# Kernel optimization log

Measured on AMD Instinct MI355X. Metric: run time of the kernel, lower is better.

## Reference

```python
import jax, jax.numpy as jnp
import numpy as np

B, L, IN, H, T = 512, 16, 128, 1024, 64


def setup_inputs() -> dict:
    key = jax.random.key(0)
    ks = jax.random.split(key, 11)
    k = 1.0 / np.sqrt(H)  # torch default init scale
    u = lambda kk, shape: jax.random.uniform(kk, shape, jnp.float32, -k, k)
    return {
        "x": jax.random.normal(ks[0], (B, L, IN), jnp.float32),
        "W_ih0": u(ks[1], (4 * H, IN)),
        "W_hh0": u(ks[2], (4 * H, H)),
        "b_ih0": u(ks[3], (4 * H,)),
        "b_hh0": u(ks[4], (4 * H,)),
        "W_ih1": u(ks[5], (4 * H, H)),
        "W_hh1": u(ks[6], (4 * H, H)),
        "b_ih1": u(ks[7], (4 * H,)),
        "b_hh1": u(ks[8], (4 * H,)),
        "W_out": u(ks[9], (IN, H)),
        "b_out": u(ks[10], (IN,)),
        "t": T,
    }


def _cell(xt, h, c, W_ih, W_hh, b_ih, b_hh):
    # PyTorch LSTM cell; gate order i, f, g, o
    g = xt @ W_ih.T + h @ W_hh.T + (b_ih + b_hh)
    i, f, gg, o = jnp.split(g, 4, axis=-1)
    c = jax.nn.sigmoid(f) * c + jax.nn.sigmoid(i) * jnp.tanh(gg)
    h = jax.nn.sigmoid(o) * jnp.tanh(c)
    return h, c


def reference(x, W_ih0, W_hh0, b_ih0, b_hh0, W_ih1, W_hh1, b_ih1, b_hh1,
              W_out, b_out, t):
    layers = ((W_ih0, W_hh0, b_ih0, b_hh0), (W_ih1, W_hh1, b_ih1, b_hh1))
    Bn = x.shape[0]
    Hn = W_hh0.shape[1]

    def stack_step(state, xt):
        new_state = []
        inp = xt
        for (h, c), p in zip(state, layers):
            h, c = _cell(inp, h, c, *p)
            new_state.append((h, c))
            inp = h
        return tuple(new_state), inp  # inp = top-layer hidden [B, H]

    z = jnp.zeros((Bn, Hn), x.dtype)
    state0 = tuple((z, z) for _ in layers)

    # prompt phase: process x over time, keep final state and last top hidden
    state, tops = jax.lax.scan(stack_step, state0, x.transpose(1, 0, 2))
    x_last = x[:, -1] + (tops[-1] @ W_out.T + b_out)  # [B, IN]

    def gen_step(carry, _):
        st, xl = carry
        st, htop = stack_step(st, xl)
        xl = xl + (htop @ W_out.T + b_out)
        return (st, xl), xl

    (_, _), gen = jax.lax.scan(gen_step, (state, x_last), None, length=t - 1)

    out = jnp.concatenate(
        [x, x_last[:, None, :], gen.transpose(1, 0, 2)], axis=1
    )  # [B, L + t, IN]
    return out
```

## Files before the change

kernel.cpp:

```cpp
#include <hip/hip_runtime.h>

#define B_    512
#define L_    16
#define IN_   128
#define H_    1024
#define T_    64
#define OUTROW 10240

#define LDC   1040
#define LDXL  144
#define RSTRIDE 67
#define RSZ   (64 * RSTRIDE)

#define KH_X  64
#define KH_H  32
#define KH_XL 4
#define KH_W0 36
#define KH_W1 64
#define KH_WO 32

typedef __attribute__((ext_vector_type(8))) short bf8;
typedef __attribute__((ext_vector_type(4))) float f4;
typedef __attribute__((ext_vector_type(4))) unsigned short us4;
typedef unsigned short u16;
typedef unsigned int   u32;

#define MFMA16(a, b, c) __builtin_amdgcn_mfma_f32_16x16x32_bf16(a, b, c, 0, 0, 0)

__device__ __forceinline__ u16 f2bf(float f) {
    u32 u = __builtin_bit_cast(u32, f);
    u32 r = (u + 0x7fffu + ((u >> 16) & 1u)) >> 16;
    return (u16)r;
}
__device__ __forceinline__ float sigm(float x) { return 1.f / (1.f + __expf(-x)); }
__device__ __forceinline__ float tanh_f(float x) {
    float ax = fabsf(x);
    float e = __expf(-2.f * ax);
    float t = (1.f - e) / (1.f + e);
    return x < 0.f ? -t : t;
}
__device__ __forceinline__ bf8 ld8(const u16* p) { return *(const bf8*)p; }

__device__ __forceinline__ size_t swz(int kh_stride, int row, int k) {
    return ((size_t)(row >> 4) * kh_stride + (k >> 5)) * 512
           + ((k & 31) >> 3) * 128 + (row & 15) * 8 + (k & 7);
}

#define MFMAP(AS, BS)                                                       \
  do {                                                                      \
    _Pragma("unroll")                                                       \
    for (int g_ = 0; g_ < 4; ++g_)                                          \
      _Pragma("unroll")                                                     \
      for (int t_ = 0; t_ < 4; ++t_)                                        \
        acc[g_][t_] = MFMA16(AS[g_], BS[t_], acc[g_][t_]);                  \
  } while (0)

#define LOADP_CELL(AS, BS, PH)                                              \
  do {                                                                      \
    const int kt_ = ws + (((PH) >> 1) << 2);                                \
    const int s_  = (PH) & 1;                                               \
    const bool ix_ = kt_ < nk1;                                             \
    const int oA_ = (((ix_ ? kt_ : kt_ - nk1) << 1) + s_) * 512;            \
    const int oB_ = ((kt_ << 1) + s_) * 512;                                \
    _Pragma("unroll")                                                       \
    for (int g_ = 0; g_ < 4; ++g_)                                          \
      AS[g_] = ld8((ix_ ? apx[g_] : aph[g_]) + oA_);                        \
    _Pragma("unroll")                                                       \
    for (int t_ = 0; t_ < 4; ++t_) BS[t_] = ld8(bp[t_] + oB_);              \
  } while (0)

#define LOADP_PROJ(AS, BS, PH)                                              \
  do {                                                                      \
    const int kt_ = ws + (((PH) >> 1) << 2);                                \
    const int o_  = ((kt_ << 1) + ((PH) & 1)) * 512;                        \
    _Pragma("unroll")                                                       \
    for (int g_ = 0; g_ < 4; ++g_) AS[g_] = ld8(ap[g_] + o_);               \
    _Pragma("unroll")                                                       \
    for (int t_ = 0; t_ < 4; ++t_) BS[t_] = ld8(bp[t_] + o_);               \
  } while (0)

__device__ __forceinline__ void cell_body(int bid,
    const u16* __restrict__ pA0, int kh0, int nk1,
    const u16* __restrict__ pA1, int kh1, int nk2,
    const u16* __restrict__ pB, int khB,
    const float* __restrict__ bias, float* __restrict__ Cst,
    u16* __restrict__ Hdst, float* __restrict__ red)
{
    const int tn = (bid & 7) * 8 + ((bid >> 3) & 7);
    const int tm = bid >> 6;
    const int tid = threadIdx.x;
    const int lane = tid & 63, ws = tid >> 6;
    const int l15 = lane & 15, qd = lane >> 4, q4 = qd * 4;

    const int erow = ws * 16 + l15;
    const int grow = tm * 64 + erow;
    const int colb = tn * 16 + q4;
    const f4 cold = *(const f4*)&Cst[(size_t)grow * LDC + colb];

    f4 acc[4][4];
#pragma unroll
    for (int i = 0; i < 4; ++i)
#pragma unroll
        for (int j = 0; j < 4; ++j) acc[i][j] = (f4)(0.f);

    const u16* bp[4];
#pragma unroll
    for (int t = 0; t < 4; ++t)
        bp[t] = pB + (size_t)(tn * 4 + t) * khB * 512 + lane * 8;
    const u16* apx[4];
    const u16* aph[4];
#pragma unroll
    for (int g = 0; g < 4; ++g) {
        apx[g] = pA0 + (size_t)(tm * 4 + g) * kh0 * 512 + lane * 8;
        aph[g] = pA1 + (size_t)(tm * 4 + g) * kh1 * 512 + lane * 8;
    }

    const int nk  = nk1 + nk2;
    const int myn = (nk - ws + 3) >> 2;
    const int nph = myn * 2;

    bf8 A0[4], B0[4], A1[4], B1[4], A2[4], B2[4], A3[4], B3[4];
    LOADP_CELL(A0, B0, 0);
    LOADP_CELL(A1, B1, 1);
    LOADP_CELL(A2, B2, 2);
    int ph = 0;
    for (; ph + 4 <= nph; ph += 4) {
        LOADP_CELL(A3, B3, ph + 3);
        MFMAP(A0, B0);
        if (ph + 4 < nph) LOADP_CELL(A0, B0, ph + 4);
        MFMAP(A1, B1);
        if (ph + 5 < nph) LOADP_CELL(A1, B1, ph + 5);
        MFMAP(A2, B2);
        if (ph + 6 < nph) LOADP_CELL(A2, B2, ph + 6);
        MFMAP(A3, B3);
    }
    if (ph < nph) {
        MFMAP(A0, B0);
        MFMAP(A1, B1);
    }

#pragma unroll
    for (int rg = 0; rg < 4; ++rg)
#pragma unroll
        for (int t = 0; t < 4; ++t)
#pragma unroll
            for (int r = 0; r < 4; ++r)
                red[ws * RSZ + (rg * 16 + q4 + r) * RSTRIDE + t * 16 + l15] = acc[rg][t][r];
    __syncthreads();

    f4 gs[4];
#pragma unroll
    for (int G = 0; G < 4; ++G) {
        f4 s;
#pragma unroll
        for (int j = 0; j < 4; ++j) {
            const int cidx = erow * RSTRIDE + G * 16 + q4 + j;
            s[j] = red[0 * RSZ + cidx] + red[1 * RSZ + cidx]
                 + red[2 * RSZ + cidx] + red[3 * RSZ + cidx];
        }
        gs[G] = s + *(const f4*)&bias[tn * 64 + G * 16 + q4];
    }
    f4 cn; us4 h4;
#pragma unroll
    for (int j = 0; j < 4; ++j) {
        const float I  = sigm(gs[0][j]);
        const float F  = sigm(gs[1][j]);
        const float Gg = tanh_f(gs[2][j]);
        const float O  = sigm(gs[3][j]);
        cn[j] = F * cold[j] + I * Gg;
        h4[j] = f2bf(O * tanh_f(cn[j]));
    }
    *(f4*)&Cst[(size_t)grow * LDC + colb] = cn;
    *(us4*)&Hdst[swz(KH_H, grow, colb)] = h4;
}

__global__ __launch_bounds__(256, 2) void cell_gemm(
    const u16* __restrict__ pA0, int kh0, int nk1,
    const u16* __restrict__ pA1, int kh1, int nk2,
    const u16* __restrict__ pB, int khB,
    const float* __restrict__ bias, float* __restrict__ Cst, u16* __restrict__ Hdst)
{
    __shared__ float red[4 * RSZ];
    cell_body(blockIdx.x, pA0, kh0, nk1, pA1, kh1, nk2, pB, khB, bias, Cst, Hdst, red);
}

__global__ __launch_bounds__(256, 2) void pair_k(
    const u16* __restrict__ A0a, int kh0a, int nk1a,
    const u16* __restrict__ A1a, int kh1a, int nk2a,
    const u16* __restrict__ Ba, int khBa,
    const float* __restrict__ ba, float* __restrict__ Ca, u16* __restrict__ Ha,
    const u16* __restrict__ A0b, int kh0b, int nk1b,
    const u16* __restrict__ A1b, int kh1b, int nk2b,
    const u16* __restrict__ Bb, int khBb,
    const float* __restrict__ bb, float* __restrict__ Cb, u16* __restrict__ Hb)
{
    __shared__ float red[4 * RSZ];
    if (blockIdx.x < 512)
        cell_body(blockIdx.x, A0a, kh0a, nk1a, A1a, kh1a, nk2a, Ba, khBa, ba, Ca, Ha, red);
    else
        cell_body(blockIdx.x - 512, A0b, kh0b, nk1b, A1b, kh1b, nk2b, Bb, khBb, bb, Cb, Hb, red);
}

__global__ __launch_bounds__(256, 2) void proj_gemm(
    const u16* __restrict__ pA,
    const u16* __restrict__ pB,
    const float* __restrict__ bout,
    const float* __restrict__ xin, int ldxin,
    float* __restrict__ XL, u16* __restrict__ XLbf,
    float* __restrict__ dout, int slot)
{
    __shared__ float red[4 * RSZ];
    const int bid = blockIdx.x;
    const int tn = bid >> 3, tm = bid & 7;
    const int tid = threadIdx.x;
    const int lane = tid & 63, ws = tid >> 6;
    const int l15 = lane & 15, qd = lane >> 4;

    f4 acc[4][4];
#pragma unroll
    for (int i = 0; i < 4; ++i)
#pragma unroll
        for (int j = 0; j < 4; ++j) acc[i][j] = (f4)(0.f);

    const u16* bp[4];
#pragma unroll
    for (int t = 0; t < 4; ++t)
        bp[t] = pB + (size_t)(tn * 4 + t) * KH_WO * 512 + lane * 8;
    const u16* ap[4];
#pragma unroll
    for (int g = 0; g < 4; ++g)
        ap[g] = pA + (size_t)(tm * 4 + g) * KH_H * 512 + lane * 8;

    const int nph = 8;
    bf8 A0[4], B0[4], A1[4], B1[4], A2[4], B2[4], A3[4], B3[4];
    LOADP_PROJ(A0, B0, 0);
    LOADP_PROJ(A1, B1, 1);
    LOADP_PROJ(A2, B2, 2);
    for (int ph = 0; ph + 4 <= nph; ph += 4) {
        LOADP_PROJ(A3, B3, ph + 3);
        MFMAP(A0, B0);
        if (ph + 4 < nph) LOADP_PROJ(A0, B0, ph + 4);
        MFMAP(A1, B1);
        if (ph + 5 < nph) LOADP_PROJ(A1, B1, ph + 5);
        MFMAP(A2, B2);
        if (ph + 6 < nph) LOADP_PROJ(A2, B2, ph + 6);
        MFMAP(A3, B3);
    }

#pragma unroll
    for (int rg = 0; rg < 4; ++rg)
#pragma unroll
        for (int t = 0; t < 4; ++t)
#pragma unroll
            for (int r = 0; r < 4; ++r)
                red[ws * RSZ + (rg * 16 + qd * 4 + r) * RSTRIDE + t * 16 + l15] = acc[rg][t][r];
    __syncthreads();

    const int erow = ws * 16 + l15;
    const int grow = tm * 64 + erow;
#pragma unroll
    for (int jb = 0; jb < 4; ++jb) {
        const int cin = qd * 16 + jb * 4;
        const int col = tn * 64 + cin;
        f4 s;
#pragma unroll
        for (int j2 = 0; j2 < 4; ++j2) {
            const int cidx = erow * RSTRIDE + cin + j2;
            s[j2] = red[0 * RSZ + cidx] + red[1 * RSZ + cidx]
                  + red[2 * RSZ + cidx] + red[3 * RSZ + cidx];
        }
        const f4 v = *(const f4*)&xin[(size_t)grow * ldxin + col] + s
                     + *(const f4*)&bout[col];
        *(f4*)&XL[(size_t)grow * LDXL + col] = v;
        us4 b;
#pragma unroll
        for (int j2 = 0; j2 < 4; ++j2) b[j2] = f2bf(v[j2]);
        *(us4*)&XLbf[swz(KH_XL, grow, col)] = b;
        *(f4*)&dout[(size_t)grow * OUTROW + slot * IN_ + col] = v;
    }
}

__global__ void conv_w(const float* Wih0, const float* Whh0, const float* bih0, const float* bhh0,
                       const float* Wih1, const float* Whh1, const float* bih1, const float* bhh1,
                       const float* Wout,
                       u16* W0c, float* b0p, u16* W1c, float* b1p, u16* Woutb)
{
    const int bid = blockIdx.x, t = threadIdx.x;
    const int lane = t >> 2;
    const int l15 = lane & 15, qd = lane >> 4;
    const int j0 = (t & 3) * 2;
    const int c0_ = qd * 8 + j0;

    if (bid < 9216) {
        const int rg = bid / 36, kh = bid - rg * 36;
        const int p = rg * 16 + l15;
        const int rem = p & 63, G = rem >> 4, u = (p >> 6) * 16 + (rem & 15);
        const int src = G * H_ + u;
        float e0, e1;
        if (kh < 4) {
            e0 = Wih0[(size_t)src * IN_ + kh * 32 + c0_];
            e1 = Wih0[(size_t)src * IN_ + kh * 32 + c0_ + 1];
        } else {
            e0 = Whh0[(size_t)src * H_ + (kh - 4) * 32 + c0_];
            e1 = Whh0[(size_t)src * H_ + (kh - 4) * 32 + c0_ + 1];
        }
        ((u32*)W0c)[(size_t)bid * 256 + t] = (u32)f2bf(e0) | ((u32)f2bf(e1) << 16);
        if (kh == 0 && qd == 0 && j0 == 0) b0p[p] = bih0[src] + bhh0[src];
    } else if (bid < 25600) {
        const int x = bid - 9216;
        const int rg = x >> 6, kh = x & 63;
        const int p = rg * 16 + l15;
        const int rem = p & 63, G = rem >> 4, u = (p >> 6) * 16 + (rem & 15);
        const int src = G * H_ + u;
        float e0, e1;
        if (kh < 32) {
            e0 = Wih1[(size_t)src * H_ + kh * 32 + c0_];
            e1 = Wih1[(size_t)src * H_ + kh * 32 + c0_ + 1];
        } else {
            e0 = Whh1[(size_t)src * H_ + (kh - 32) * 32 + c0_];
            e1 = Whh1[(size_t)src * H_ + (kh - 32) * 32 + c0_ + 1];
        }
        ((u32*)W1c)[(size_t)x * 256 + t] = (u32)f2bf(e0) | ((u32)f2bf(e1) << 16);
        if (kh == 0 && qd == 0 && j0 == 0) b1p[p] = bih1[src] + bhh1[src];
    } else {
        const int x = bid - 25600;
        const int rg = x >> 5, kh = x & 31;
        const int r = rg * 16 + l15;
        const float e0 = Wout[(size_t)r * H_ + kh * 32 + c0_];
        const float e1 = Wout[(size_t)r * H_ + kh * 32 + c0_ + 1];
        ((u32*)Woutb)[(size_t)x * 256 + t] = (u32)f2bf(e0) | ((u32)f2bf(e1) << 16);
    }
}

__global__ void setup_k(const float* __restrict__ x, u16* __restrict__ Xb,
                        u16* H0, u16* H1, float* c0, float* c1,
                        float* __restrict__ dout)
{
    const int i = blockIdx.x * 256 + threadIdx.x;
    const float v = x[i];
    const int r = i >> 11, col = i & 2047;
    Xb[swz(KH_X, r, col)] = f2bf(v);
    dout[(size_t)r * OUTROW + col] = v;
    if (i < B_ * H_) {
        H0[i] = 0; H1[i] = 0;
        const int rr = i >> 10, cc = i & 1023;
        c0[(size_t)rr * LDC + cc] = 0.f; c1[(size_t)rr * LDC + cc] = 0.f;
    }
}

extern "C" void kernel_launch(void* const* d_in, const int* in_sizes, int n_in,
                              void* d_out, int out_size, void* d_ws, size_t ws_size,
                              hipStream_t stream)
{
    const float* x    = (const float*)d_in[0];
    const float* Wih0 = (const float*)d_in[1];
    const float* Whh0 = (const float*)d_in[2];
    const float* bih0 = (const float*)d_in[3];
    const float* bhh0 = (const float*)d_in[4];
    const float* Wih1 = (const float*)d_in[5];
    const float* Whh1 = (const float*)d_in[6];
    const float* bih1 = (const float*)d_in[7];
    const float* bhh1 = (const float*)d_in[8];
    const float* Wout = (const float*)d_in[9];
    const float* bout = (const float*)d_in[10];
    float* dout = (float*)d_out;

    char* ws = (char*)d_ws;
    size_t off = 0;
    auto alloc = [&](size_t bytes) -> char* {
        char* p = ws + off; off += (bytes + 255) & ~(size_t)255; return p;
    };
    u16*  W0c   = (u16*)alloc((size_t)9216 * 1024);
    u16*  W1c   = (u16*)alloc((size_t)16384 * 1024);
    u16*  Woutb = (u16*)alloc((size_t)256 * 1024);
    float* b0p  = (float*)alloc(4096 * 4);
    float* b1p  = (float*)alloc(4096 * 4);
    u16*  Xb    = (u16*)alloc((size_t)2048 * 1024);
    u16*  H0b[2]; H0b[0] = (u16*)alloc((size_t)1024 * 1024); H0b[1] = (u16*)alloc((size_t)1024 * 1024);
    u16*  H1b[2]; H1b[0] = (u16*)alloc((size_t)1024 * 1024); H1b[1] = (u16*)alloc((size_t)1024 * 1024);
    float* c0   = (float*)alloc((size_t)B_ * LDC * 4);
    float* c1   = (float*)alloc((size_t)B_ * LDC * 4);
    float* XL   = (float*)alloc((size_t)B_ * LDXL * 4);
    u16*  XLbf  = (u16*)alloc((size_t)128 * 1024);

    conv_w<<<25856, 256, 0, stream>>>(Wih0, Whh0, bih0, bhh0,
                                      Wih1, Whh1, bih1, bhh1, Wout,
                                      W0c, b0p, W1c, b1p, Woutb);
    setup_k<<<4096, 256, 0, stream>>>(x, Xb, H0b[0], H1b[0], c0, c1, dout);

    int p = 0;
    cell_gemm<<<512, 256, 0, stream>>>(Xb, KH_X, 2, H0b[0], KH_H, 16,
                                       W0c, KH_W0, b0p, c0, H0b[1]);
    for (int g = 0; g < 15; ++g) {
        pair_k<<<1024, 256, 0, stream>>>(
            H0b[1 - p], KH_H, 16, H1b[p], KH_H, 16, W1c, KH_W1, b1p, c1, H1b[1 - p],
            Xb + (size_t)(g + 1) * 2048, KH_X, 2, H0b[1 - p], KH_H, 16,
            W0c, KH_W0, b0p, c0, H0b[p]);
        p ^= 1;
    }
    cell_gemm<<<512, 256, 0, stream>>>(H0b[0], KH_H, 16, H1b[1], KH_H, 16,
                                       W1c, KH_W1, b1p, c1, H1b[0]);
    proj_gemm<<<16, 256, 0, stream>>>(H1b[0], Woutb, bout,
                                      x + 15 * IN_, L_ * IN_, XL, XLbf, dout, 16);

    p = 0;
    for (int g = 16; g < 79; ++g) {
        cell_gemm<<<512, 256, 0, stream>>>(XLbf, KH_XL, 2, H0b[p], KH_H, 16,
                                           W0c, KH_W0, b0p, c0, H0b[1 - p]);
        cell_gemm<<<512, 256, 0, stream>>>(H0b[1 - p], KH_H, 16, H1b[p], KH_H, 16,
                                           W1c, KH_W1, b1p, c1, H1b[1 - p]);
        const int s = g - 15;
        proj_gemm<<<16, 256, 0, stream>>>(H1b[1 - p], Woutb, bout,
                                          XL, LDXL, XL, XLbf, dout, 16 + s);
        p ^= 1;
    }
}
```

Measured before the change: 2.623 ms.

## Fuse layer-1 cell and output projection into one kernel with per-row-tile counters

Merges the layer-1 LSTM cell GEMM and the output projection into one launch. The 64 projection blocks spin on per-row-tile atomic counters until the 64 cell blocks producing that tile's hidden state have finished. The projection is also re-tiled from 16 blocks with 64x64 tiles into 64 blocks with 16x64 tiles, giving more parallelism and a smaller register footprint. This saves a launch and a serial tail each step. The risks are spin-wait deadlock if the spinning blocks take CUs before the producer blocks run, and memory-ordering hazards.

Result: slower. 3.355 ms (+27.9%).

```diff
diff --git a/kernel.cpp b/kernel.cpp
--- a/kernel.cpp
+++ b/kernel.cpp
@@ -11,6 +11,7 @@
 #define LDXL  144
 #define RSTRIDE 67
 #define RSZ   (64 * RSTRIDE)
+#define PRST  68
 
 #define KH_X  64
 #define KH_H  32
@@ -69,22 +70,12 @@
     for (int t_ = 0; t_ < 4; ++t_) BS[t_] = ld8(bp[t_] + oB_);              \
   } while (0)
 
-#define LOADP_PROJ(AS, BS, PH)                                              \
-  do {                                                                      \
-    const int kt_ = ws + (((PH) >> 1) << 2);                                \
-    const int o_  = ((kt_ << 1) + ((PH) & 1)) * 512;                        \
-    _Pragma("unroll")                                                       \
-    for (int g_ = 0; g_ < 4; ++g_) AS[g_] = ld8(ap[g_] + o_);               \
-    _Pragma("unroll")                                                       \
-    for (int t_ = 0; t_ < 4; ++t_) BS[t_] = ld8(bp[t_] + o_);               \
-  } while (0)
-
 __device__ __forceinline__ void cell_body(int bid,
     const u16* __restrict__ pA0, int kh0, int nk1,
     const u16* __restrict__ pA1, int kh1, int nk2,
     const u16* __restrict__ pB, int khB,
     const float* __restrict__ bias, float* __restrict__ Cst,
-    u16* __restrict__ Hdst, float* __restrict__ red)
+    u16* Hdst, float* __restrict__ red)
 {
     const int tn = (bid & 7) * 8 + ((bid >> 3) & 7);
     const int tm = bid >> 6;
@@ -201,83 +192,101 @@
         cell_body(blockIdx.x - 512, A0b, kh0b, nk1b, A1b, kh1b, nk2b, Bb, khBb, bb, Cb, Hb, red);
 }
 
-__global__ __launch_bounds__(256, 2) void proj_gemm(
-    const u16* __restrict__ pA,
+__global__ __launch_bounds__(256, 2) void fused_k(
+    const u16* __restrict__ pA0, const u16* __restrict__ pA1,
     const u16* __restrict__ pB,
+    const float* __restrict__ bias, float* __restrict__ Cst, u16* Hdst,
+    const u16* pH1,
+    const u16* __restrict__ pWo,
     const float* __restrict__ bout,
     const float* __restrict__ xin, int ldxin,
     float* __restrict__ XL, u16* __restrict__ XLbf,
-    float* __restrict__ dout, int slot)
+    float* __restrict__ dout, int slot,
+    u32* cnt, u32 target)
 {
     __shared__ float red[4 * RSZ];
     const int bid = blockIdx.x;
-    const int tn = bid >> 3, tm = bid & 7;
     const int tid = threadIdx.x;
+
+    if (bid < 512) {
+        cell_body(bid, pA0, KH_H, 16, pA1, KH_H, 16, pB, KH_W1,
+                  bias, Cst, Hdst, red);
+        __syncthreads();
+        if (tid == 0) {
+            __threadfence();
+            atomicAdd(&cnt[(bid >> 6) * 32], 1u);
+        }
+        return;
+    }
+
+    const int pb = bid - 512;
+    const int tn = pb & 1, tmq = pb >> 1;
+    const int tm = tmq >> 2;
     const int lane = tid & 63, ws = tid >> 6;
     const int l15 = lane & 15, qd = lane >> 4;
 
-    f4 acc[4][4];
-#pragma unroll
-    for (int i = 0; i < 4; ++i)
-#pragma unroll
-        for (int j = 0; j < 4; ++j) acc[i][j] = (f4)(0.f);
-
+    if (tid == 0) {
+        while (__hip_atomic_load(&cnt[tm * 32], __ATOMIC_ACQUIRE,
+                                 __HIP_MEMORY_SCOPE_AGENT) < target)
+            __builtin_amdgcn_s_sleep(8);
+        __threadfence();
+    }
+    __syncthreads();
+
+    f4 acc[4];
+#pragma unroll
+    for (int t = 0; t < 4; ++t) acc[t] = (f4)(0.f);
+
+    const u16* ap = pH1 + (size_t)tmq * KH_H * 512 + lane * 8;
     const u16* bp[4];
 #pragma unroll
     for (int t = 0; t < 4; ++t)
-        bp[t] = pB + (size_t)(tn * 4 + t) * KH_WO * 512 + lane * 8;
-    const u16* ap[4];
-#pragma unroll
-    for (int g = 0; g < 4; ++g)
-        ap[g] = pA + (size_t)(tm * 4 + g) * KH_H * 512 + lane * 8;
-
-    const int nph = 8;
-    bf8 A0[4], B0[4], A1[4], B1[4], A2[4], B2[4], A3[4], B3[4];
-    LOADP_PROJ(A0, B0, 0);
-    LOADP_PROJ(A1, B1, 1);
-    LOADP_PROJ(A2, B2, 2);
-    for (int ph = 0; ph + 4 <= nph; ph += 4) {
-        LOADP_PROJ(A3, B3, ph + 3);
-        MFMAP(A0, B0);
-        if (ph + 4 < nph) LOADP_PROJ(A0, B0, ph + 4);
-        MFMAP(A1, B1);
-        if (ph + 5 < nph) LOADP_PROJ(A1, B1, ph + 5);
-        MFMAP(A2, B2);
-        if (ph + 6 < nph) LOADP_PROJ(A2, B2, ph + 6);
-        MFMAP(A3, B3);
-    }
-
-#pragma unroll
-    for (int rg = 0; rg < 4; ++rg)
-#pragma unroll
-        for (int t = 0; t < 4; ++t)
-#pragma unroll
-            for (int r = 0; r < 4; ++r)
-                red[ws * RSZ + (rg * 16 + qd * 4 + r) * RSTRIDE + t * 16 + l15] = acc[rg][t][r];
+        bp[t] = pWo + (size_t)(tn * 4 + t) * KH_WO * 512 + lane * 8;
+
+    bf8 A0, B0[4], A1, B1[4];
+#define LOADP_P(AV, BV, PH)                                                 \
+    do {                                                                    \
+        const int kt_ = ws + (((PH) >> 1) << 2);                            \
+        const int o_  = ((kt_ << 1) + ((PH) & 1)) * 512;                    \
+        AV = ld8(ap + o_);                                                  \
+        _Pragma("unroll")                                                   \
+        for (int t_ = 0; t_ < 4; ++t_) BV[t_] = ld8(bp[t_] + o_);           \
+    } while (0)
+
+    LOADP_P(A0, B0, 0);
+    for (int ph = 0; ph < 8; ph += 2) {
+        LOADP_P(A1, B1, ph + 1);
+#pragma unroll
+        for (int t = 0; t < 4; ++t) acc[t] = MFMA16(A0, B0[t], acc[t]);
+        if (ph + 2 < 8) LOADP_P(A0, B0, ph + 2);
+#pragma unroll
+        for (int t = 0; t < 4; ++t) acc[t] = MFMA16(A1, B1[t], acc[t]);
+    }
+#undef LOADP_P
+
+#pragma unroll
+    for (int t = 0; t < 4; ++t)
+#pragma unroll
+        for (int r = 0; r < 4; ++r)
+            red[ws * (16 * PRST) + (qd * 4 + r) * PRST + t * 16 + l15] = acc[t][r];
     __syncthreads();
 
-    const int erow = ws * 16 + l15;
-    const int grow = tm * 64 + erow;
-#pragma unroll
-    for (int jb = 0; jb < 4; ++jb) {
-        const int cin = qd * 16 + jb * 4;
-        const int col = tn * 64 + cin;
-        f4 s;
-#pragma unroll
-        for (int j2 = 0; j2 < 4; ++j2) {
-            const int cidx = erow * RSTRIDE + cin + j2;
-            s[j2] = red[0 * RSZ + cidx] + red[1 * RSZ + cidx]
-                  + red[2 * RSZ + cidx] + red[3 * RSZ + cidx];
-        }
-        const f4 v = *(const f4*)&xin[(size_t)grow * ldxin + col] + s
-                     + *(const f4*)&bout[col];
-        *(f4*)&XL[(size_t)grow * LDXL + col] = v;
-        us4 b;
-#pragma unroll
-        for (int j2 = 0; j2 < 4; ++j2) b[j2] = f2bf(v[j2]);
-        *(us4*)&XLbf[swz(KH_XL, grow, col)] = b;
-        *(f4*)&dout[(size_t)grow * OUTROW + slot * IN_ + col] = v;
-    }
+    const int row = tid >> 4;
+    const int cq  = (tid & 15) * 4;
+    const int col = tn * 64 + cq;
+    const int grow = tmq * 16 + row;
+    f4 s = (f4)(0.f);
+#pragma unroll
+    for (int w = 0; w < 4; ++w)
+        s += *(const f4*)&red[w * (16 * PRST) + row * PRST + cq];
+    const f4 v = *(const f4*)&xin[(size_t)grow * ldxin + col] + s
+                 + *(const f4*)&bout[col];
+    *(f4*)&XL[(size_t)grow * LDXL + col] = v;
+    us4 b;
+#pragma unroll
+    for (int j = 0; j < 4; ++j) b[j] = f2bf(v[j]);
+    *(us4*)&XLbf[swz(KH_XL, grow, col)] = b;
+    *(f4*)&dout[(size_t)grow * OUTROW + slot * IN_ + col] = v;
 }
 
 __global__ void conv_w(const float* Wih0, const float* Whh0, const float* bih0, const float* bhh0,
@@ -334,9 +343,10 @@
 
 __global__ void setup_k(const float* __restrict__ x, u16* __restrict__ Xb,
                         u16* H0, u16* H1, float* c0, float* c1,
-                        float* __restrict__ dout)
+                        float* __restrict__ dout, u32* cnt)
 {
     const int i = blockIdx.x * 256 + threadIdx.x;
+    if (i < 256) cnt[i] = 0;
     const float v = x[i];
     const int r = i >> 11, col = i & 2047;
     Xb[swz(KH_X, r, col)] = f2bf(v);
@@ -382,11 +392,12 @@
     float* c1   = (float*)alloc((size_t)B_ * LDC * 4);
     float* XL   = (float*)alloc((size_t)B_ * LDXL * 4);
     u16*  XLbf  = (u16*)alloc((size_t)128 * 1024);
+    u32*  cnt   = (u32*)alloc(256 * 4);
 
     conv_w<<<25856, 256, 0, stream>>>(Wih0, Whh0, bih0, bhh0,
                                       Wih1, Whh1, bih1, bhh1, Wout,
                                       W0c, b0p, W1c, b1p, Woutb);
-    setup_k<<<4096, 256, 0, stream>>>(x, Xb, H0b[0], H1b[0], c0, c1, dout);
+    setup_k<<<4096, 256, 0, stream>>>(x, Xb, H0b[0], H1b[0], c0, c1, dout, cnt);
 
     int p = 0;
     cell_gemm<<<512, 256, 0, stream>>>(Xb, KH_X, 2, H0b[0], KH_H, 16,
@@ -398,20 +409,20 @@
             W0c, KH_W0, b0p, c0, H0b[p]);
         p ^= 1;
     }
-    cell_gemm<<<512, 256, 0, stream>>>(H0b[0], KH_H, 16, H1b[1], KH_H, 16,
-                                       W1c, KH_W1, b1p, c1, H1b[0]);
-    proj_gemm<<<16, 256, 0, stream>>>(H1b[0], Woutb, bout,
-                                      x + 15 * IN_, L_ * IN_, XL, XLbf, dout, 16);
+    fused_k<<<576, 256, 0, stream>>>(H0b[0], H1b[1], W1c, b1p, c1, H1b[0],
+                                     H1b[0], Woutb, bout,
+                                     x + 15 * IN_, L_ * IN_, XL, XLbf, dout, 16,
+                                     cnt, 64u * 1);
 
     p = 0;
     for (int g = 16; g < 79; ++g) {
         cell_gemm<<<512, 256, 0, stream>>>(XLbf, KH_XL, 2, H0b[p], KH_H, 16,
                                            W0c, KH_W0, b0p, c0, H0b[1 - p]);
-        cell_gemm<<<512, 256, 0, stream>>>(H0b[1 - p], KH_H, 16, H1b[p], KH_H, 16,
-                                           W1c, KH_W1, b1p, c1, H1b[1 - p]);
         const int s = g - 15;
-        proj_gemm<<<16, 256, 0, stream>>>(H1b[1 - p], Woutb, bout,
-                                          XL, LDXL, XL, XLbf, dout, 16 + s);
+        fused_k<<<576, 256, 0, stream>>>(H0b[1 - p], H1b[p], W1c, b1p, c1, H1b[1 - p],
+                                         H1b[1 - p], Woutb, bout,
+                                         XL, LDXL, XL, XLbf, dout, 16 + s,
+                                         cnt, 64u * (u32)(s + 1));
         p ^= 1;
     }
 }
```

## Fold output projection into layer-0 input via precomputed Wih0·Wout and running preactivation

Applied to the files above, without the earlier changes.

Layer 0's input-gate preactivation during rollout is kept as a running fp32 buffer P. Because x_last grows by W_out·h_top + b_out each step, P is advanced by (Wih0·Wout)·h_top + Wih0·b_out, using a combined weight precomputed once. The standalone projection GEMM is folded into the layer-0 cell kernel, where 2 of 64 column tiles compute it, and the small-K XL input GEMM is removed. This cuts one launch per step and shortens the dependency chain, but adds a 4096x1024 combined-weight GEMM operand, a P read-modify-write, and bf16 rounding of the combined weight, which may change accuracy.

New measurement: 3.250 ms. 23.9% more time.

```diff
diff --git a/kernel.cpp b/kernel.cpp
--- a/kernel.cpp
+++ b/kernel.cpp
@@ -9,12 +9,12 @@
 
 #define LDC   1040
 #define LDXL  144
+#define LDP   4112
 #define RSTRIDE 67
 #define RSZ   (64 * RSTRIDE)
 
 #define KH_X  64
 #define KH_H  32
-#define KH_XL 4
 #define KH_W0 36
 #define KH_W1 64
 #define KH_WO 32
@@ -46,14 +46,15 @@
            + ((k & 31) >> 3) * 128 + (row & 15) * 8 + (k & 7);
 }
 
-#define MFMAP(AS, BS)                                                       \
+#define MFMAPX(ACC, AS, BS)                                                 \
   do {                                                                      \
     _Pragma("unroll")                                                       \
     for (int g_ = 0; g_ < 4; ++g_)                                          \
       _Pragma("unroll")                                                     \
       for (int t_ = 0; t_ < 4; ++t_)                                        \
-        acc[g_][t_] = MFMA16(AS[g_], BS[t_], acc[g_][t_]);                  \
+        ACC[g_][t_] = MFMA16(AS[g_], BS[t_], ACC[g_][t_]);                  \
   } while (0)
+#define MFMAP(AS, BS) MFMAPX(acc, AS, BS)
 
 #define LOADP_CELL(AS, BS, PH)                                              \
   do {                                                                      \
@@ -67,16 +68,6 @@
       AS[g_] = ld8((ix_ ? apx[g_] : aph[g_]) + oA_);                        \
     _Pragma("unroll")                                                       \
     for (int t_ = 0; t_ < 4; ++t_) BS[t_] = ld8(bp[t_] + oB_);              \
-  } while (0)
-
-#define LOADP_PROJ(AS, BS, PH)                                              \
-  do {                                                                      \
-    const int kt_ = ws + (((PH) >> 1) << 2);                                \
-    const int o_  = ((kt_ << 1) + ((PH) & 1)) * 512;                        \
-    _Pragma("unroll")                                                       \
-    for (int g_ = 0; g_ < 4; ++g_) AS[g_] = ld8(ap[g_] + o_);               \
-    _Pragma("unroll")                                                       \
-    for (int t_ = 0; t_ < 4; ++t_) BS[t_] = ld8(bp[t_] + o_);               \
   } while (0)
 
 __device__ __forceinline__ void cell_body(int bid,
@@ -201,83 +192,244 @@
         cell_body(blockIdx.x - 512, A0b, kh0b, nk1b, A1b, kh1b, nk2b, Bb, khBb, bb, Cb, Hb, red);
 }
 
-__global__ __launch_bounds__(256, 2) void proj_gemm(
-    const u16* __restrict__ pA,
-    const u16* __restrict__ pB,
-    const float* __restrict__ bout,
-    const float* __restrict__ xin, int ldxin,
-    float* __restrict__ XL, u16* __restrict__ XLbf,
-    float* __restrict__ dout, int slot)
+__global__ __launch_bounds__(256, 2) void cellA_k(
+    const u16* __restrict__ pH1, const u16* __restrict__ pH0,
+    const u16* __restrict__ pWc, const u16* __restrict__ pW0,
+    const float* __restrict__ b0p_, const float* __restrict__ bc0,
+    float* __restrict__ P, float* __restrict__ Cst, u16* __restrict__ Hdst,
+    const u16* __restrict__ pWo, const float* __restrict__ bout_,
+    float* __restrict__ XL, float* __restrict__ dout, int slot)
 {
     __shared__ float red[4 * RSZ];
     const int bid = blockIdx.x;
-    const int tn = bid >> 3, tm = bid & 7;
+    const int tn = (bid & 7) * 8 + ((bid >> 3) & 7);
+    const int tm = bid >> 6;
     const int tid = threadIdx.x;
     const int lane = tid & 63, ws = tid >> 6;
-    const int l15 = lane & 15, qd = lane >> 4;
-
-    f4 acc[4][4];
-#pragma unroll
-    for (int i = 0; i < 4; ++i)
-#pragma unroll
-        for (int j = 0; j < 4; ++j) acc[i][j] = (f4)(0.f);
-
-    const u16* bp[4];
-#pragma unroll
-    for (int t = 0; t < 4; ++t)
-        bp[t] = pB + (size_t)(tn * 4 + t) * KH_WO * 512 + lane * 8;
-    const u16* ap[4];
-#pragma unroll
-    for (int g = 0; g < 4; ++g)
-        ap[g] = pA + (size_t)(tm * 4 + g) * KH_H * 512 + lane * 8;
-
-    const int nph = 8;
-    bf8 A0[4], B0[4], A1[4], B1[4], A2[4], B2[4], A3[4], B3[4];
-    LOADP_PROJ(A0, B0, 0);
-    LOADP_PROJ(A1, B1, 1);
-    LOADP_PROJ(A2, B2, 2);
-    for (int ph = 0; ph + 4 <= nph; ph += 4) {
-        LOADP_PROJ(A3, B3, ph + 3);
-        MFMAP(A0, B0);
-        if (ph + 4 < nph) LOADP_PROJ(A0, B0, ph + 4);
-        MFMAP(A1, B1);
-        if (ph + 5 < nph) LOADP_PROJ(A1, B1, ph + 5);
-        MFMAP(A2, B2);
-        if (ph + 6 < nph) LOADP_PROJ(A2, B2, ph + 6);
-        MFMAP(A3, B3);
-    }
-
-#pragma unroll
-    for (int rg = 0; rg < 4; ++rg)
-#pragma unroll
-        for (int t = 0; t < 4; ++t)
-#pragma unroll
-            for (int r = 0; r < 4; ++r)
-                red[ws * RSZ + (rg * 16 + qd * 4 + r) * RSTRIDE + t * 16 + l15] = acc[rg][t][r];
-    __syncthreads();
+    const int l15 = lane & 15, qd = lane >> 4, q4 = qd * 4;
 
     const int erow = ws * 16 + l15;
     const int grow = tm * 64 + erow;
-#pragma unroll
-    for (int jb = 0; jb < 4; ++jb) {
-        const int cin = qd * 16 + jb * 4;
-        const int col = tn * 64 + cin;
+    const int colb = tn * 16 + q4;
+    const f4 cold = *(const f4*)&Cst[(size_t)grow * LDC + colb];
+
+    if (tn < 2) {
+        f4 pacc[4][4];
+#pragma unroll
+        for (int i = 0; i < 4; ++i)
+#pragma unroll
+            for (int j = 0; j < 4; ++j) pacc[i][j] = (f4)(0.f);
+        const u16* pap[4];
+        const u16* pbp[4];
+#pragma unroll
+        for (int g = 0; g < 4; ++g)
+            pap[g] = pH1 + (size_t)(tm * 4 + g) * (KH_H * 512) + lane * 8;
+#pragma unroll
+        for (int t = 0; t < 4; ++t)
+            pbp[t] = pWo + (size_t)(tn * 4 + t) * (KH_WO * 512) + lane * 8;
+#define LOADQ(AS, BS, PH)                                                   \
+  { const int o_ = (((ws + (((PH) >> 1) << 2)) << 1) + ((PH) & 1)) * 512;   \
+    _Pragma("unroll")                                                       \
+    for (int g_ = 0; g_ < 4; ++g_) AS[g_] = ld8(pap[g_] + o_);              \
+    _Pragma("unroll")                                                       \
+    for (int t_ = 0; t_ < 4; ++t_) BS[t_] = ld8(pbp[t_] + o_); }
+        bf8 A0[4], B0[4], A1[4], B1[4];
+        LOADQ(A0, B0, 0);
+        for (int ph = 0; ph < 8; ph += 2) {
+            LOADQ(A1, B1, ph + 1);
+            MFMAPX(pacc, A0, B0);
+            if (ph + 2 < 8) LOADQ(A0, B0, ph + 2);
+            MFMAPX(pacc, A1, B1);
+        }
+#undef LOADQ
+#pragma unroll
+        for (int rg = 0; rg < 4; ++rg)
+#pragma unroll
+            for (int t = 0; t < 4; ++t)
+#pragma unroll
+                for (int r = 0; r < 4; ++r)
+                    red[ws * RSZ + (rg * 16 + q4 + r) * RSTRIDE + t * 16 + l15] = pacc[rg][t][r];
+        __syncthreads();
+#pragma unroll
+        for (int jb = 0; jb < 4; ++jb) {
+            const int cin = qd * 16 + jb * 4;
+            const int col = tn * 64 + cin;
+            f4 s;
+#pragma unroll
+            for (int j2 = 0; j2 < 4; ++j2) {
+                const int cidx = erow * RSTRIDE + cin + j2;
+                s[j2] = red[0 * RSZ + cidx] + red[1 * RSZ + cidx]
+                      + red[2 * RSZ + cidx] + red[3 * RSZ + cidx];
+            }
+            const f4 v = *(const f4*)&XL[(size_t)grow * LDXL + col] + s
+                         + *(const f4*)&bout_[col];
+            *(f4*)&XL[(size_t)grow * LDXL + col] = v;
+            *(f4*)&dout[(size_t)grow * OUTROW + slot * IN_ + col] = v;
+        }
+        __syncthreads();
+    }
+
+    const int half = ws >> 1, wl = ws & 1;
+    const u16* ap[4];
+    const u16* bp[4];
+#pragma unroll
+    for (int g = 0; g < 4; ++g)
+        ap[g] = (half ? pH0 : pH1) + (size_t)(tm * 4 + g) * (KH_H * 512) + lane * 8;
+#pragma unroll
+    for (int t = 0; t < 4; ++t)
+        bp[t] = half ? pW0 + (size_t)(tn * 4 + t) * (KH_W0 * 512) + 4 * 512 + lane * 8
+                     : pWc + (size_t)(tn * 4 + t) * (KH_H * 512) + lane * 8;
+
+    f4 acc[4][4];
+#pragma unroll
+    for (int i = 0; i < 4; ++i)
+#pragma unroll
+        for (int j = 0; j < 4; ++j) acc[i][j] = (f4)(0.f);
+
+#define LOADA(AS, BS, PH)                                                   \
+  { const int kt_ = wl + (((PH) >> 1) << 1);                                \
+    const int o_ = ((kt_ << 1) + ((PH) & 1)) * 512;                         \
+    _Pragma("unroll")                                                       \
+    for (int g_ = 0; g_ < 4; ++g_) AS[g_] = ld8(ap[g_] + o_);               \
+    _Pragma("unroll")                                                       \
+    for (int t_ = 0; t_ < 4; ++t_) BS[t_] = ld8(bp[t_] + o_); }
+
+    bf8 A0[4], B0[4], A1[4], B1[4], A2[4], B2[4], A3[4], B3[4];
+    LOADA(A0, B0, 0);
+    LOADA(A1, B1, 1);
+    LOADA(A2, B2, 2);
+    for (int ph = 0; ph + 4 <= 16; ph += 4) {
+        LOADA(A3, B3, ph + 3);
+        MFMAP(A0, B0);
+        if (ph + 4 < 16) LOADA(A0, B0, ph + 4);
+        MFMAP(A1, B1);
+        if (ph + 5 < 16) LOADA(A1, B1, ph + 5);
+        MFMAP(A2, B2);
+        if (ph + 6 < 16) LOADA(A2, B2, ph + 6);
+        MFMAP(A3, B3);
+    }
+#undef LOADA
+
+#pragma unroll
+    for (int rg = 0; rg < 4; ++rg)
+#pragma unroll
+        for (int t = 0; t < 4; ++t)
+#pragma unroll
+            for (int r = 0; r < 4; ++r)
+                red[ws * RSZ + (rg * 16 + q4 + r) * RSTRIDE + t * 16 + l15] = acc[rg][t][r];
+    __syncthreads();
+
+    f4 gs[4];
+#pragma unroll
+    for (int G = 0; G < 4; ++G) {
+        f4 pinc, hp;
+#pragma unroll
+        for (int j = 0; j < 4; ++j) {
+            const int cidx = erow * RSTRIDE + G * 16 + q4 + j;
+            pinc[j] = red[0 * RSZ + cidx] + red[1 * RSZ + cidx];
+            hp[j]   = red[2 * RSZ + cidx] + red[3 * RSZ + cidx];
+        }
+        const int pc = tn * 64 + G * 16 + q4;
+        const f4 pold = *(const f4*)&P[(size_t)grow * LDP + pc];
+        const f4 pnew = pold + pinc + *(const f4*)&bc0[pc];
+        *(f4*)&P[(size_t)grow * LDP + pc] = pnew;
+        gs[G] = pnew + hp + *(const f4*)&b0p_[pc];
+    }
+    f4 cn; us4 h4;
+#pragma unroll
+    for (int j = 0; j < 4; ++j) {
+        const float I  = sigm(gs[0][j]);
+        const float F  = sigm(gs[1][j]);
+        const float Gg = tanh_f(gs[2][j]);
+        const float O  = sigm(gs[3][j]);
+        cn[j] = F * cold[j] + I * Gg;
+        h4[j] = f2bf(O * tanh_f(cn[j]));
+    }
+    *(f4*)&Cst[(size_t)grow * LDC + colb] = cn;
+    *(us4*)&Hdst[swz(KH_H, grow, colb)] = h4;
+}
+
+__global__ __launch_bounds__(256, 2) void pinit_k(
+    const u16* __restrict__ pXb, const u16* __restrict__ pW0,
+    float* __restrict__ P)
+{
+    __shared__ float red[4 * RSZ];
+    const int bid = blockIdx.x;
+    const int tn = (bid & 7) * 8 + ((bid >> 3) & 7);
+    const int tm = bid >> 6;
+    const int tid = threadIdx.x;
+    const int lane = tid & 63, ws = tid >> 6;
+    const int l15 = lane & 15, qd = lane >> 4, q4 = qd * 4;
+
+    f4 acc[4][4];
+#pragma unroll
+    for (int i = 0; i < 4; ++i)
+#pragma unroll
+        for (int j = 0; j < 4; ++j) acc[i][j] = (f4)(0.f);
+
+    bf8 A[4], B[4];
+#pragma unroll
+    for (int g = 0; g < 4; ++g)
+        A[g] = ld8(pXb + ((size_t)(tm * 4 + g) * KH_X + 60 + ws) * 512 + lane * 8);
+#pragma unroll
+    for (int t = 0; t < 4; ++t)
+        B[t] = ld8(pW0 + ((size_t)(tn * 4 + t) * KH_W0 + ws) * 512 + lane * 8);
+    MFMAP(A, B);
+
+#pragma unroll
+    for (int rg = 0; rg < 4; ++rg)
+#pragma unroll
+        for (int t = 0; t < 4; ++t)
+#pragma unroll
+            for (int r = 0; r < 4; ++r)
+                red[ws * RSZ + (rg * 16 + q4 + r) * RSTRIDE + t * 16 + l15] = acc[rg][t][r];
+    __syncthreads();
+
+    const int erow = ws * 16 + l15;
+    const int grow = tm * 64 + erow;
+#pragma unroll
+    for (int G = 0; G < 4; ++G) {
         f4 s;
 #pragma unroll
-        for (int j2 = 0; j2 < 4; ++j2) {
-            const int cidx = erow * RSTRIDE + cin + j2;
-            s[j2] = red[0 * RSZ + cidx] + red[1 * RSZ + cidx]
-                  + red[2 * RSZ + cidx] + red[3 * RSZ + cidx];
-        }
-        const f4 v = *(const f4*)&xin[(size_t)grow * ldxin + col] + s
-                     + *(const f4*)&bout[col];
-        *(f4*)&XL[(size_t)grow * LDXL + col] = v;
-        us4 b;
-#pragma unroll
-        for (int j2 = 0; j2 < 4; ++j2) b[j2] = f2bf(v[j2]);
-        *(us4*)&XLbf[swz(KH_XL, grow, col)] = b;
-        *(f4*)&dout[(size_t)grow * OUTROW + slot * IN_ + col] = v;
-    }
+        for (int j = 0; j < 4; ++j) {
+            const int cidx = erow * RSTRIDE + G * 16 + q4 + j;
+            s[j] = red[0 * RSZ + cidx] + red[1 * RSZ + cidx]
+                 + red[2 * RSZ + cidx] + red[3 * RSZ + cidx];
+        }
+        *(f4*)&P[(size_t)grow * LDP + tn * 64 + G * 16 + q4] = s;
+    }
+}
+
+__global__ void wcomb_k(const float* __restrict__ Wih0, const float* __restrict__ Wout,
+                        u16* __restrict__ Wc)
+{
+    const int idx = blockIdx.x * 256 + threadIdx.x;
+    const int h = idx & 1023, p0 = (idx >> 10) << 2;
+    const int rem = p0 & 63, G = rem >> 4, u0 = (p0 >> 6) * 16 + (rem & 15);
+    const int src0 = G * H_ + u0;
+    float s0 = 0.f, s1 = 0.f, s2 = 0.f, s3 = 0.f;
+    for (int i = 0; i < IN_; ++i) {
+        const float wv = Wout[(size_t)i * H_ + h];
+        s0 += wv * Wih0[(size_t)(src0 + 0) * IN_ + i];
+        s1 += wv * Wih0[(size_t)(src0 + 1) * IN_ + i];
+        s2 += wv * Wih0[(size_t)(src0 + 2) * IN_ + i];
+        s3 += wv * Wih0[(size_t)(src0 + 3) * IN_ + i];
+    }
+    Wc[swz(KH_H, p0 + 0, h)] = f2bf(s0);
+    Wc[swz(KH_H, p0 + 1, h)] = f2bf(s1);
+    Wc[swz(KH_H, p0 + 2, h)] = f2bf(s2);
+    Wc[swz(KH_H, p0 + 3, h)] = f2bf(s3);
+}
+
+__global__ void bc0_k(const float* __restrict__ Wih0, const float* __restrict__ bout_,
+                      float* __restrict__ bc0)
+{
+    const int p = blockIdx.x * 256 + threadIdx.x;
+    const int rem = p & 63, G = rem >> 4, u = (p >> 6) * 16 + (rem & 15);
+    const int src = G * H_ + u;
+    float s = 0.f;
+    for (int i = 0; i < IN_; ++i) s += bout_[i] * Wih0[(size_t)src * IN_ + i];
+    bc0[p] = s;
 }
 
 __global__ void conv_w(const float* Wih0, const float* Whh0, const float* bih0, const float* bhh0,
@@ -334,13 +486,14 @@
 
 __global__ void setup_k(const float* __restrict__ x, u16* __restrict__ Xb,
                         u16* H0, u16* H1, float* c0, float* c1,
-                        float* __restrict__ dout)
+                        float* __restrict__ dout, float* __restrict__ XL)
 {
     const int i = blockIdx.x * 256 + threadIdx.x;
     const float v = x[i];
     const int r = i >> 11, col = i & 2047;
     Xb[swz(KH_X, r, col)] = f2bf(v);
     dout[(size_t)r * OUTROW + col] = v;
+    if (col >= 1920) XL[(size_t)r * LDXL + col - 1920] = v;
     if (i < B_ * H_) {
         H0[i] = 0; H1[i] = 0;
         const int rr = i >> 10, cc = i & 1023;
@@ -373,20 +526,25 @@
     u16*  W0c   = (u16*)alloc((size_t)9216 * 1024);
     u16*  W1c   = (u16*)alloc((size_t)16384 * 1024);
     u16*  Woutb = (u16*)alloc((size_t)256 * 1024);
+    u16*  Wcomb = (u16*)alloc((size_t)8192 * 1024);
     float* b0p  = (float*)alloc(4096 * 4);
     float* b1p  = (float*)alloc(4096 * 4);
+    float* bc0  = (float*)alloc(4096 * 4);
     u16*  Xb    = (u16*)alloc((size_t)2048 * 1024);
     u16*  H0b[2]; H0b[0] = (u16*)alloc((size_t)1024 * 1024); H0b[1] = (u16*)alloc((size_t)1024 * 1024);
     u16*  H1b[2]; H1b[0] = (u16*)alloc((size_t)1024 * 1024); H1b[1] = (u16*)alloc((size_t)1024 * 1024);
     float* c0   = (float*)alloc((size_t)B_ * LDC * 4);
     float* c1   = (float*)alloc((size_t)B_ * LDC * 4);
     float* XL   = (float*)alloc((size_t)B_ * LDXL * 4);
-    u16*  XLbf  = (u16*)alloc((size_t)128 * 1024);
+    float* P    = (float*)alloc((size_t)B_ * LDP * 4);
 
     conv_w<<<25856, 256, 0, stream>>>(Wih0, Whh0, bih0, bhh0,
                                       Wih1, Whh1, bih1, bhh1, Wout,
                                       W0c, b0p, W1c, b1p, Woutb);
-    setup_k<<<4096, 256, 0, stream>>>(x, Xb, H0b[0], H1b[0], c0, c1, dout);
+    wcomb_k<<<4096, 256, 0, stream>>>(Wih0, Wout, Wcomb);
+    bc0_k<<<16, 256, 0, stream>>>(Wih0, bout, bc0);
+    setup_k<<<4096, 256, 0, stream>>>(x, Xb, H0b[0], H1b[0], c0, c1, dout, XL);
+    pinit_k<<<512, 256, 0, stream>>>(Xb, W0c, P);
 
     int p = 0;
     cell_gemm<<<512, 256, 0, stream>>>(Xb, KH_X, 2, H0b[0], KH_H, 16,
@@ -400,18 +558,14 @@
     }
     cell_gemm<<<512, 256, 0, stream>>>(H0b[0], KH_H, 16, H1b[1], KH_H, 16,
                                        W1c, KH_W1, b1p, c1, H1b[0]);
-    proj_gemm<<<16, 256, 0, stream>>>(H1b[0], Woutb, bout,
-                                      x + 15 * IN_, L_ * IN_, XL, XLbf, dout, 16);
-
-    p = 0;
-    for (int g = 16; g < 79; ++g) {
-        cell_gemm<<<512, 256, 0, stream>>>(XLbf, KH_XL, 2, H0b[p], KH_H, 16,
-                                           W0c, KH_W0, b0p, c0, H0b[1 - p]);
-        cell_gemm<<<512, 256, 0, stream>>>(H0b[1 - p], KH_H, 16, H1b[p], KH_H, 16,
-                                           W1c, KH_W1, b1p, c1, H1b[1 - p]);
-        const int s = g - 15;
-        proj_gemm<<<16, 256, 0, stream>>>(H1b[1 - p], Woutb, bout,
-                                          XL, LDXL, XL, XLbf, dout, 16 + s);
-        p ^= 1;
-    }
-}
+
+    for (int s = 0; s < 64; ++s) {
+        cellA_k<<<512, 256, 0, stream>>>(H1b[s & 1], H0b[s & 1], Wcomb, W0c,
+                                         b0p, bc0, P, c0, H0b[1 - (s & 1)],
+                                         Woutb, bout, XL, dout, 16 + s);
+        if (s < 63)
+            cell_gemm<<<512, 256, 0, stream>>>(H0b[1 - (s & 1)], KH_H, 16,
+                                               H1b[s & 1], KH_H, 16,
+                                               W1c, KH_W1, b1p, c1, H1b[1 - (s & 1)]);
+    }
+}
```
